# Kernel tuning notes

Measured on AMD Instinct MI355X. Metric: run time of the kernel, lower is better.

Reference implementation:

```python
import jax, jax.numpy as jnp
import numpy as np

D = 1024
H = 16
HD = D // H
N_TEXT = 256
N_VISION = 256
N_FRAMES = 12


def setup_inputs() -> dict:
    key = jax.random.key(0)
    ks = jax.random.split(key, 10)
    s = 1.0 / np.sqrt(D)
    return {
        "text_hidden_states": jax.random.normal(ks[0], (N_TEXT, D), jnp.float32),
        "vision_hidden_states": jax.random.normal(ks[1], (N_VISION, N_FRAMES, D), jnp.float32),
        "wq": jax.random.normal(ks[2], (D, D), jnp.float32) * s,
        "bq": jnp.zeros((D,), jnp.float32),
        "wk": jax.random.normal(ks[3], (D, D), jnp.float32) * s,
        "bk": jnp.zeros((D,), jnp.float32),
        "wv": jax.random.normal(ks[4], (D, D), jnp.float32) * s,
        "bv": jnp.zeros((D,), jnp.float32),
        "wo": jax.random.normal(ks[5], (D, D), jnp.float32) * s,
        "bo": jnp.zeros((D,), jnp.float32),
    }


def reference(text_hidden_states, vision_hidden_states, wq, bq, wk, bk, wv, bv, wo, bo):
    n_text = text_hidden_states.shape[0]
    n_vision, n_frames, _ = vision_hidden_states.shape
    # projections (torch Linear: x @ W.T + b)
    q = (text_hidden_states @ wq.T + bq).reshape(n_text, H, HD)            # [t,h,d]
    k = (vision_hidden_states @ wk.T + bk).reshape(n_vision, n_frames, H, HD)  # [v,f,h,d]
    v = (vision_hidden_states @ wv.T + bv).reshape(n_vision, n_frames, H, HD)  # [v,f,h,d]
    # shared query broadcast over vision batch: scores [v,h,f,t]
    scores = jnp.einsum("vfhd,thd->vhft", k, q) / jnp.sqrt(jnp.asarray(HD, scores_dtype := q.dtype))
    probs = jax.nn.softmax(scores, axis=2)  # softmax over frames (dim=2)
    # attn_output [v,t,h,d] -> [v,t,D]
    out = jnp.einsum("vfhd,vhft->vthd", v, probs).reshape(n_vision, n_text, D)
    return out @ wo.T + bo
```

## Files before the change

### kernel.cpp

```cpp
#include <hip/hip_runtime.h>

typedef short bf16x8 __attribute__((ext_vector_type(8)));
typedef float f32x4 __attribute__((ext_vector_type(4)));

__device__ __forceinline__ unsigned short f2bf(float f) {
  union { float f; unsigned u; } x; x.f = f;
  unsigned u = x.u;
  u += 0x7fffu + ((u >> 16) & 1u);
  return (unsigned short)(u >> 16);
}

__global__ __launch_bounds__(256) void cvt_all(
    const float* __restrict__ text, const float* __restrict__ vis,
    const float* __restrict__ wq, const float* __restrict__ wk,
    const float* __restrict__ wv, const float* __restrict__ wo,
    unsigned short* __restrict__ o0, unsigned short* __restrict__ o1,
    unsigned short* __restrict__ o2, unsigned short* __restrict__ o3,
    unsigned short* __restrict__ o4, unsigned short* __restrict__ o5)
{
  long i4 = (long)blockIdx.x * 256 + threadIdx.x;
  const float* src; unsigned short* dst; long base;
  if      (i4 <   65536) { src = text; dst = o0; base = 0; }
  else if (i4 <  851968) { src = vis;  dst = o1; base = 65536; }
  else if (i4 < 1114112) { src = wq;   dst = o2; base = 851968; }
  else if (i4 < 1376256) { src = wk;   dst = o3; base = 1114112; }
  else if (i4 < 1638400) { src = wv;   dst = o4; base = 1376256; }
  else                   { src = wo;   dst = o5; base = 1638400; }
  long li = i4 - base;
  float4 f = reinterpret_cast<const float4*>(src)[li];
  uint2 u;
  u.x = (unsigned)f2bf(f.x) | ((unsigned)f2bf(f.y) << 16);
  u.y = (unsigned)f2bf(f.z) | ((unsigned)f2bf(f.w) << 16);
  reinterpret_cast<uint2*>(dst)[li] = u;
}

__global__ __launch_bounds__(256) void gemm_abt_bf16(
    const unsigned short* __restrict__ A,
    const unsigned short* __restrict__ B,
    unsigned short* __restrict__ C,
    const float* __restrict__ bias,
    int K, int lda, int ldb, int ldc)
{
  __shared__ unsigned short As[64][40];
  __shared__ unsigned short Bs[64][40];
  const int m0 = blockIdx.y * 64, n0 = blockIdx.x * 64;
  const int tid = threadIdx.x;
  const int lane = tid & 63, w = tid >> 6;
  const int wm = w >> 1, wn = w & 1;
  const int r16 = lane & 15, kg = lane >> 4;
  const int srow = tid >> 2, sseg = tid & 3;

  const f32x4 fzero = {0.f, 0.f, 0.f, 0.f};
  f32x4 acc[2][2];
#pragma unroll
  for (int i = 0; i < 2; ++i)
#pragma unroll
    for (int j = 0; j < 2; ++j) acc[i][j] = fzero;

  for (int k0 = 0; k0 < K; k0 += 32) {
    __syncthreads();
    *reinterpret_cast<int4*>(&As[srow][sseg * 8]) =
        *reinterpret_cast<const int4*>(&A[(long)(m0 + srow) * lda + k0 + sseg * 8]);
    *reinterpret_cast<int4*>(&Bs[srow][sseg * 8]) =
        *reinterpret_cast<const int4*>(&B[(long)(n0 + srow) * ldb + k0 + sseg * 8]);
    __syncthreads();
    bf16x8 a[2], b[2];
#pragma unroll
    for (int i = 0; i < 2; ++i)
      a[i] = *reinterpret_cast<const bf16x8*>(&As[wm * 32 + i * 16 + r16][kg * 8]);
#pragma unroll
    for (int j = 0; j < 2; ++j)
      b[j] = *reinterpret_cast<const bf16x8*>(&Bs[wn * 32 + j * 16 + r16][kg * 8]);
#pragma unroll
    for (int i = 0; i < 2; ++i)
#pragma unroll
      for (int j = 0; j < 2; ++j)
        acc[i][j] = __builtin_amdgcn_mfma_f32_16x16x32_bf16(a[i], b[j], acc[i][j], 0, 0, 0);
  }
#pragma unroll
  for (int i = 0; i < 2; ++i) {
#pragma unroll
    for (int j = 0; j < 2; ++j) {
      const int row = m0 + wm * 32 + i * 16 + kg * 4;
      const int col = n0 + wn * 32 + j * 16 + r16;
      const float bv = bias ? bias[col] : 0.f;
#pragma unroll
      for (int r = 0; r < 4; ++r)
        C[(long)(row + r) * ldc + col] = f2bf(acc[i][j][r] + bv);
    }
  }
}

__global__ __launch_bounds__(256) void gemm_abt_bf16_kv(
    const unsigned short* __restrict__ A,
    const unsigned short* __restrict__ B0,
    const unsigned short* __restrict__ B1,
    unsigned short* __restrict__ C0,
    unsigned short* __restrict__ C1,
    const float* __restrict__ bias0,
    const float* __restrict__ bias1,
    int K, int lda, int ldb, int ldc)
{
  const unsigned short* B = blockIdx.z ? B1 : B0;
  unsigned short* C = blockIdx.z ? C1 : C0;
  const float* bias = blockIdx.z ? bias1 : bias0;

  __shared__ unsigned short As[64][40];
  __shared__ unsigned short Bs[64][40];
  const int m0 = blockIdx.y * 64, n0 = blockIdx.x * 64;
  const int tid = threadIdx.x;
  const int lane = tid & 63, w = tid >> 6;
  const int wm = w >> 1, wn = w & 1;
  const int r16 = lane & 15, kg = lane >> 4;
  const int srow = tid >> 2, sseg = tid & 3;

  const f32x4 fzero = {0.f, 0.f, 0.f, 0.f};
  f32x4 acc[2][2];
#pragma unroll
  for (int i = 0; i < 2; ++i)
#pragma unroll
    for (int j = 0; j < 2; ++j) acc[i][j] = fzero;

  for (int k0 = 0; k0 < K; k0 += 32) {
    __syncthreads();
    *reinterpret_cast<int4*>(&As[srow][sseg * 8]) =
        *reinterpret_cast<const int4*>(&A[(long)(m0 + srow) * lda + k0 + sseg * 8]);
    *reinterpret_cast<int4*>(&Bs[srow][sseg * 8]) =
        *reinterpret_cast<const int4*>(&B[(long)(n0 + srow) * ldb + k0 + sseg * 8]);
    __syncthreads();
    bf16x8 a[2], b[2];
#pragma unroll
    for (int i = 0; i < 2; ++i)
      a[i] = *reinterpret_cast<const bf16x8*>(&As[wm * 32 + i * 16 + r16][kg * 8]);
#pragma unroll
    for (int j = 0; j < 2; ++j)
      b[j] = *reinterpret_cast<const bf16x8*>(&Bs[wn * 32 + j * 16 + r16][kg * 8]);
#pragma unroll
    for (int i = 0; i < 2; ++i)
#pragma unroll
      for (int j = 0; j < 2; ++j)
        acc[i][j] = __builtin_amdgcn_mfma_f32_16x16x32_bf16(a[i], b[j], acc[i][j], 0, 0, 0);
  }
#pragma unroll
  for (int i = 0; i < 2; ++i) {
#pragma unroll
    for (int j = 0; j < 2; ++j) {
      const int row = m0 + wm * 32 + i * 16 + kg * 4;
      const int col = n0 + wn * 32 + j * 16 + r16;
      const float bv = bias ? bias[col] : 0.f;
#pragma unroll
      for (int r = 0; r < 4; ++r)
        C[(long)(row + r) * ldc + col] = f2bf(acc[i][j][r] + bv);
    }
  }
}

__global__ __launch_bounds__(256) void scores_softmax(
    const unsigned short* __restrict__ Kp,
    const unsigned short* __restrict__ Qp,
    unsigned short* __restrict__ P)
{
  const int h = blockIdx.x, v = blockIdx.y;
  const int tid = threadIdx.x, lane = tid & 63, w = tid >> 6;
  const int r16 = lane & 15, kg = lane >> 4;
  __shared__ unsigned short Ks[16][72];
  __shared__ unsigned short Qs[256][72];

  if (tid < 96) {
    const int f = tid >> 3, seg = tid & 7;
    *reinterpret_cast<int4*>(&Ks[f][seg * 8]) =
        *reinterpret_cast<const int4*>(&Kp[(long)(v * 12 + f) * 1024 + h * 64 + seg * 8]);
  } else if (tid < 128) {
    const int f = 12 + ((tid - 96) >> 3), seg = (tid - 96) & 7;
    int4 z; z.x = 0; z.y = 0; z.z = 0; z.w = 0;
    *reinterpret_cast<int4*>(&Ks[f][seg * 8]) = z;
  }
#pragma unroll
  for (int rep = 0; rep < 8; ++rep) {
    const int row = rep * 32 + (tid >> 3), seg = tid & 7;
    *reinterpret_cast<int4*>(&Qs[row][seg * 8]) =
        *reinterpret_cast<const int4*>(&Qp[(long)row * 1024 + h * 64 + seg * 8]);
  }
  __syncthreads();

  const f32x4 fzero = {0.f, 0.f, 0.f, 0.f};
  f32x4 acc[4];
#pragma unroll
  for (int j = 0; j < 4; ++j) acc[j] = fzero;

#pragma unroll
  for (int kk = 0; kk < 64; kk += 32) {
    bf16x8 a = *reinterpret_cast<const bf16x8*>(&Ks[r16][kk + kg * 8]);
#pragma unroll
    for (int j = 0; j < 4; ++j) {
      bf16x8 b = *reinterpret_cast<const bf16x8*>(&Qs[w * 64 + j * 16 + r16][kk + kg * 8]);
      acc[j] = __builtin_amdgcn_mfma_f32_16x16x32_bf16(a, b, acc[j], 0, 0, 0);
    }
  }
#pragma unroll
  for (int j = 0; j < 4; ++j) {
    float lm = -1e30f;
    if (kg < 3) {
#pragma unroll
      for (int r = 0; r < 4; ++r) lm = fmaxf(lm, acc[j][r] * 0.125f);
    }
    lm = fmaxf(lm, __shfl_xor(lm, 16));
    lm = fmaxf(lm, __shfl_xor(lm, 32));
    float p[4]; float ls = 0.f;
    if (kg < 3) {
#pragma unroll
      for (int r = 0; r < 4; ++r) { p[r] = __expf(acc[j][r] * 0.125f - lm); ls += p[r]; }
    }
    ls += __shfl_xor(ls, 16);
    ls += __shfl_xor(ls, 32);
    const float inv = 1.f / ls;
    if (kg < 3) {
      const int t = w * 64 + j * 16 + r16;
#pragma unroll
      for (int r = 0; r < 4; ++r)
        P[((long)v * 256 + t) * 192 + (kg * 4 + r) * 16 + h] = f2bf(p[r] * inv);
    }
  }
}

__global__ __launch_bounds__(256) void combine(
    const unsigned short* __restrict__ VPp,
    const unsigned short* __restrict__ Wo,
    const unsigned short* __restrict__ P,
    const float* __restrict__ bo,
    float* __restrict__ out)
{
  const int wgid = blockIdx.x;
  const int xcd = wgid & 7, idx = wgid >> 3;
  const int v = ((idx & 31) << 3) | xcd;
  const int n0 = (idx >> 5) << 6;

  const int tid = threadIdx.x, lane = tid & 63, w = tid >> 6;
  const int r16 = lane & 15, kg = lane >> 4;

  __shared__ unsigned short BsAll[64 * 192];

  const unsigned short* VPv = VPp + (long)v * 12 * 1024;
#pragma unroll
  for (int hi = 0; hi < 4; ++hi) {
    const int h = (w << 2) + hi;
    const int db = h * 64;
    f32x4 accp[4] = {{0.f,0.f,0.f,0.f},{0.f,0.f,0.f,0.f},{0.f,0.f,0.f,0.f},{0.f,0.f,0.f,0.f}};
#pragma unroll
    for (int kk = 0; kk < 64; kk += 32) {
      bf16x8 a = {0,0,0,0,0,0,0,0};
      if (r16 < 12)
        a = *reinterpret_cast<const bf16x8*>(&VPv[(long)r16 * 1024 + db + kk + kg * 8]);
      bf16x8 bfr[4];
#pragma unroll
      for (int j = 0; j < 4; ++j)
        bfr[j] = *reinterpret_cast<const bf16x8*>(
            &Wo[(long)(n0 + j * 16 + r16) * 1024 + db + kk + kg * 8]);
#pragma unroll
      for (int j = 0; j < 4; ++j)
        accp[j] = __builtin_amdgcn_mfma_f32_16x16x32_bf16(a, bfr[j], accp[j], 0, 0, 0);
    }
#pragma unroll
    for (int j = 0; j < 4; ++j) {
#pragma unroll
      for (int r = 0; r < 4; ++r) {
        const int f = kg * 4 + r;
        if (f < 12) {
          const int o = j * 16 + r16;
          const int k = f * 16 + h;
          BsAll[o * 192 + (((k >> 3) ^ (o & 7)) << 3) + (k & 7)] = f2bf(accp[j][r]);
        }
      }
    }
  }

  const unsigned short* Pv = P + (long)v * 256 * 192;
  bf16x8 aP[4];
#pragma unroll
  for (int i = 0; i < 4; ++i)
    aP[i] = *reinterpret_cast<const bf16x8*>(
        &Pv[(long)(w * 64 + i * 16 + r16) * 192 + kg * 8]);

  __syncthreads();

  f32x4 acc[4][4];
#pragma unroll
  for (int i = 0; i < 4; ++i)
#pragma unroll
    for (int j = 0; j < 4; ++j) { f32x4 z = {0.f,0.f,0.f,0.f}; acc[i][j] = z; }

#pragma unroll
  for (int k0 = 0; k0 < 192; k0 += 32) {
    bf16x8 aC[4];
#pragma unroll
    for (int i = 0; i < 4; ++i) aC[i] = aP[i];
    if (k0 < 160) {
#pragma unroll
      for (int i = 0; i < 4; ++i)
        aP[i] = *reinterpret_cast<const bf16x8*>(
            &Pv[(long)(w * 64 + i * 16 + r16) * 192 + (k0 + 32) + kg * 8]);
    }
    bf16x8 b[4];
#pragma unroll
    for (int j = 0; j < 4; ++j) {
      const int row = j * 16 + r16;
      const int slot = (k0 >> 3) + kg;
      b[j] = *reinterpret_cast<const bf16x8*>(
          &BsAll[row * 192 + ((slot ^ (row & 7)) << 3)]);
    }
#pragma unroll
    for (int i = 0; i < 4; ++i)
#pragma unroll
      for (int j = 0; j < 4; ++j)
        acc[i][j] = __builtin_amdgcn_mfma_f32_16x16x32_bf16(aC[i], b[j], acc[i][j], 0, 0, 0);
  }
#pragma unroll
  for (int i = 0; i < 4; ++i) {
#pragma unroll
    for (int j = 0; j < 4; ++j) {
      const int trow = w * 64 + i * 16 + kg * 4;
      const int col = n0 + j * 16 + r16;
      const float bv = bo[col];
#pragma unroll
      for (int r = 0; r < 4; ++r)
        out[((long)v * 256 + trow + r) * 1024 + col] = acc[i][j][r] + bv;
    }
  }
}

extern "C" void kernel_launch(void* const* d_in, const int* in_sizes, int n_in,
                              void* d_out, int out_size, void* d_ws, size_t ws_size,
                              hipStream_t stream) {
  const float* text = (const float*)d_in[0];
  const float* vis  = (const float*)d_in[1];
  const float* wq   = (const float*)d_in[2];
  const float* bq   = (const float*)d_in[3];
  const float* wk   = (const float*)d_in[4];
  const float* bk   = (const float*)d_in[5];
  const float* wv   = (const float*)d_in[6];
  const float* bv   = (const float*)d_in[7];
  const float* wo   = (const float*)d_in[8];
  const float* bo   = (const float*)d_in[9];
  float* out = (float*)d_out;

  unsigned short* text16 = (unsigned short*)d_ws;
  unsigned short* vis16  = text16 + 262144;
  unsigned short* wq16   = vis16  + 3145728;
  unsigned short* wk16   = wq16   + 1048576;
  unsigned short* wv16   = wk16   + 1048576;
  unsigned short* wo16   = wv16   + 1048576;
  unsigned short* q16    = wo16   + 1048576;
  unsigned short* k16    = q16    + 262144;
  unsigned short* vp16   = k16    + 3145728;
  unsigned short* P      = vp16   + 3145728;

  cvt_all<<<7424, 256, 0, stream>>>(text, vis, wq, wk, wv, wo,
                                    text16, vis16, wq16, wk16, wv16, wo16);
  gemm_abt_bf16<<<dim3(16, 4), 256, 0, stream>>>(text16, wq16, q16, bq, 1024, 1024, 1024, 1024);
  gemm_abt_bf16_kv<<<dim3(16, 48, 2), 256, 0, stream>>>(
      vis16, wk16, wv16, k16, vp16, bk, bv, 1024, 1024, 1024, 1024);
  scores_softmax<<<dim3(16, 256), 256, 0, stream>>>(k16, q16, P);
  combine<<<4096, 256, 0, stream>>>(vp16, wo16, P, bo, out);
}
```

Measured before the change: 273.3 us.

## Split fused combine kernel into Z-projection and output GEMM kernels via workspace

The fused combine kernel is split into two kernels. zh_kernel computes the per-head V·Wo product and writes it to a global Z buffer. out_gemm reloads Z into LDS and multiplies it by P, prefetching the P fragments two stages ahead and storing the output with nontemporal stores. The split is meant to lower register and LDS pressure and raise occupancy in each phase, at the cost of an extra global round-trip for Z (up to 100MB) and a possible chunked loop when the workspace is small.

```diff
diff --git a/kernel.cpp b/kernel.cpp
--- a/kernel.cpp
+++ b/kernel.cpp
@@ -223,17 +223,17 @@
   }
 }
 
-__global__ __launch_bounds__(256) void combine(
+__global__ __launch_bounds__(256) void zh_kernel(
     const unsigned short* __restrict__ VPp,
     const unsigned short* __restrict__ Wo,
-    const unsigned short* __restrict__ P,
-    const float* __restrict__ bo,
-    float* __restrict__ out)
+    unsigned short* __restrict__ Z,
+    int vbase, int vsh)
 {
   const int wgid = blockIdx.x;
   const int xcd = wgid & 7, idx = wgid >> 3;
-  const int v = ((idx & 31) << 3) | xcd;
-  const int n0 = (idx >> 5) << 6;
+  const int vlocal = ((idx & ((1 << vsh) - 1)) << 3) | xcd;
+  const int v = vbase + vlocal;
+  const int n0 = (idx >> vsh) << 6;
 
   const int tid = threadIdx.x, lane = tid & 63, w = tid >> 6;
   const int r16 = lane & 15, kg = lane >> 4;
@@ -273,40 +273,81 @@
       }
     }
   }
-
+  __syncthreads();
+  unsigned short* Zv = Z + ((long)vlocal * 1024 + n0) * 192;
+  const int row = tid >> 2;
+#pragma unroll
+  for (int rep = 0; rep < 6; ++rep) {
+    const int slot = (tid & 3) + (rep << 2);
+    *reinterpret_cast<int4*>(&Zv[(long)row * 192 + slot * 8]) =
+        *reinterpret_cast<const int4*>(&BsAll[row * 192 + ((slot ^ (row & 7)) << 3)]);
+  }
+}
+
+__global__ __launch_bounds__(256) void out_gemm(
+    const unsigned short* __restrict__ Z,
+    const unsigned short* __restrict__ P,
+    const float* __restrict__ bo,
+    float* __restrict__ out,
+    int vbase, int vsh)
+{
+  const int wgid = blockIdx.x;
+  const int xcd = wgid & 7, idx = wgid >> 3;
+  const int vlocal = ((idx & ((1 << vsh) - 1)) << 3) | xcd;
+  const int v = vbase + vlocal;
+  const int n0 = (idx >> vsh) << 6;
+
+  const int tid = threadIdx.x, lane = tid & 63, w = tid >> 6;
+  const int r16 = lane & 15, kg = lane >> 4;
+
+  __shared__ unsigned short Zs[64 * 192];
+
+  const unsigned short* Zv = Z + ((long)vlocal * 1024 + n0) * 192;
+  {
+    const int row = tid >> 2;
+#pragma unroll
+    for (int rep = 0; rep < 6; ++rep) {
+      const int slot = (tid & 3) + (rep << 2);
+      *reinterpret_cast<int4*>(&Zs[row * 192 + ((slot ^ (row & 7)) << 3)]) =
+          *reinterpret_cast<const int4*>(&Zv[(long)row * 192 + slot * 8]);
+    }
+  }
   const unsigned short* Pv = P + (long)v * 256 * 192;
-  bf16x8 aP[4];
+  bf16x8 aP[2][4];
+#pragma unroll
+  for (int s = 0; s < 2; ++s)
+#pragma unroll
+    for (int i = 0; i < 4; ++i)
+      aP[s][i] = *reinterpret_cast<const bf16x8*>(
+          &Pv[(long)(w * 64 + i * 16 + r16) * 192 + s * 32 + kg * 8]);
+
+  __syncthreads();
+
+  f32x4 acc[4][4];
 #pragma unroll
   for (int i = 0; i < 4; ++i)
-    aP[i] = *reinterpret_cast<const bf16x8*>(
-        &Pv[(long)(w * 64 + i * 16 + r16) * 192 + kg * 8]);
-
-  __syncthreads();
-
-  f32x4 acc[4][4];
-#pragma unroll
-  for (int i = 0; i < 4; ++i)
 #pragma unroll
     for (int j = 0; j < 4; ++j) { f32x4 z = {0.f,0.f,0.f,0.f}; acc[i][j] = z; }
 
 #pragma unroll
-  for (int k0 = 0; k0 < 192; k0 += 32) {
-    bf16x8 aC[4];
-#pragma unroll
-    for (int i = 0; i < 4; ++i) aC[i] = aP[i];
-    if (k0 < 160) {
-#pragma unroll
-      for (int i = 0; i < 4; ++i)
-        aP[i] = *reinterpret_cast<const bf16x8*>(
-            &Pv[(long)(w * 64 + i * 16 + r16) * 192 + (k0 + 32) + kg * 8]);
-    }
+  for (int s = 0; s < 6; ++s) {
+    const int k0 = s * 32;
     bf16x8 b[4];
 #pragma unroll
     for (int j = 0; j < 4; ++j) {
       const int row = j * 16 + r16;
       const int slot = (k0 >> 3) + kg;
       b[j] = *reinterpret_cast<const bf16x8*>(
-          &BsAll[row * 192 + ((slot ^ (row & 7)) << 3)]);
+          &Zs[row * 192 + ((slot ^ (row & 7)) << 3)]);
+    }
+    bf16x8 aC[4];
+#pragma unroll
+    for (int i = 0; i < 4; ++i) aC[i] = aP[s & 1][i];
+    if (s < 4) {
+#pragma unroll
+      for (int i = 0; i < 4; ++i)
+        aP[s & 1][i] = *reinterpret_cast<const bf16x8*>(
+            &Pv[(long)(w * 64 + i * 16 + r16) * 192 + (k0 + 64) + kg * 8]);
     }
 #pragma unroll
     for (int i = 0; i < 4; ++i)
@@ -323,7 +364,8 @@
       const float bv = bo[col];
 #pragma unroll
       for (int r = 0; r < 4; ++r)
-        out[((long)v * 256 + trow + r) * 1024 + col] = acc[i][j][r] + bv;
+        __builtin_nontemporal_store(acc[i][j][r] + bv,
+            &out[((long)v * 256 + trow + r) * 1024 + col]);
     }
   }
 }
@@ -353,6 +395,13 @@
   unsigned short* k16    = q16    + 262144;
   unsigned short* vp16   = k16    + 3145728;
   unsigned short* P      = vp16   + 3145728;
+  unsigned short* Zbuf   = P     + 12582912;
+  const size_t base_shorts = 26738688;
+
+  size_t avail_shorts = (ws_size / 2 > base_shorts) ? (ws_size / 2 - base_shorts) : 0;
+  int vchunk = 256;
+  while (vchunk > 8 && (size_t)vchunk * 1024 * 192 > avail_shorts) vchunk >>= 1;
+  int vsh = 0; { int t = vchunk >> 3; while (t > 1) { t >>= 1; ++vsh; } }
 
   cvt_all<<<7424, 256, 0, stream>>>(text, vis, wq, wk, wv, wo,
                                     text16, vis16, wq16, wk16, wv16, wo16);
@@ -360,5 +409,8 @@
   gemm_abt_bf16_kv<<<dim3(16, 48, 2), 256, 0, stream>>>(
       vis16, wk16, wv16, k16, vp16, bk, bv, 1024, 1024, 1024, 1024);
   scores_softmax<<<dim3(16, 256), 256, 0, stream>>>(k16, q16, P);
-  combine<<<4096, 256, 0, stream>>>(vp16, wo16, P, bo, out);
-}
+  for (int vb = 0; vb < 256; vb += vchunk) {
+    zh_kernel<<<16 * vchunk, 256, 0, stream>>>(vp16, wo16, Zbuf, vb, vsh);
+    out_gemm<<<16 * vchunk, 256, 0, stream>>>(Zbuf, P, bo, out, vb, vsh);
+  }
+}
```

Measured after the change: 318.1 us. 1.16x slower.

## Vectorize P stores, double-buffer P loads, stage output through LDS for wide stores

Applied to the files above, without the earlier changes.

Reorders the frame/head index inside the P and staged Wo·V buffers from f*16+h to h*12+f, so each thread's four probabilities are written with one 8-byte store instead of four scattered 2-byte stores. The combine kernel now prefetches P two K-steps ahead using a two-slot register buffer. The epilogue stages accumulators through LDS per wave so it can write output rows as contiguous 16-byte nontemporal stores with vector bias, replacing scalar strided stores. This costs extra LDS traffic, extra registers and a barrier, and it relies on the wave-local staging being correctly ordered by the lgkmcnt waits.

```diff
diff --git a/kernel.cpp b/kernel.cpp
--- a/kernel.cpp
+++ b/kernel.cpp
@@ -216,9 +216,10 @@
     const float inv = 1.f / ls;
     if (kg < 3) {
       const int t = w * 64 + j * 16 + r16;
-#pragma unroll
-      for (int r = 0; r < 4; ++r)
-        P[((long)v * 256 + t) * 192 + (kg * 4 + r) * 16 + h] = f2bf(p[r] * inv);
+      uint2 u2;
+      u2.x = (unsigned)f2bf(p[0] * inv) | ((unsigned)f2bf(p[1] * inv) << 16);
+      u2.y = (unsigned)f2bf(p[2] * inv) | ((unsigned)f2bf(p[3] * inv) << 16);
+      *reinterpret_cast<uint2*>(&P[((long)v * 256 + t) * 192 + h * 12 + kg * 4]) = u2;
     }
   }
 }
@@ -267,7 +268,7 @@
         const int f = kg * 4 + r;
         if (f < 12) {
           const int o = j * 16 + r16;
-          const int k = f * 16 + h;
+          const int k = h * 12 + f;
           BsAll[o * 192 + (((k >> 3) ^ (o & 7)) << 3) + (k & 7)] = f2bf(accp[j][r]);
         }
       }
@@ -275,31 +276,25 @@
   }
 
   const unsigned short* Pv = P + (long)v * 256 * 192;
-  bf16x8 aP[4];
+  bf16x8 aP[2][4];
+#pragma unroll
+  for (int s = 0; s < 2; ++s)
+#pragma unroll
+    for (int i = 0; i < 4; ++i)
+      aP[s][i] = *reinterpret_cast<const bf16x8*>(
+          &Pv[(long)(w * 64 + i * 16 + r16) * 192 + s * 32 + kg * 8]);
+
+  __syncthreads();
+
+  f32x4 acc[4][4];
 #pragma unroll
   for (int i = 0; i < 4; ++i)
-    aP[i] = *reinterpret_cast<const bf16x8*>(
-        &Pv[(long)(w * 64 + i * 16 + r16) * 192 + kg * 8]);
-
-  __syncthreads();
-
-  f32x4 acc[4][4];
-#pragma unroll
-  for (int i = 0; i < 4; ++i)
 #pragma unroll
     for (int j = 0; j < 4; ++j) { f32x4 z = {0.f,0.f,0.f,0.f}; acc[i][j] = z; }
 
 #pragma unroll
-  for (int k0 = 0; k0 < 192; k0 += 32) {
-    bf16x8 aC[4];
-#pragma unroll
-    for (int i = 0; i < 4; ++i) aC[i] = aP[i];
-    if (k0 < 160) {
-#pragma unroll
-      for (int i = 0; i < 4; ++i)
-        aP[i] = *reinterpret_cast<const bf16x8*>(
-            &Pv[(long)(w * 64 + i * 16 + r16) * 192 + (k0 + 32) + kg * 8]);
-    }
+  for (int s = 0; s < 6; ++s) {
+    const int k0 = s * 32;
     bf16x8 b[4];
 #pragma unroll
     for (int j = 0; j < 4; ++j) {
@@ -308,23 +303,47 @@
       b[j] = *reinterpret_cast<const bf16x8*>(
           &BsAll[row * 192 + ((slot ^ (row & 7)) << 3)]);
     }
+    bf16x8 aC[4];
+#pragma unroll
+    for (int i = 0; i < 4; ++i) aC[i] = aP[s & 1][i];
+    if (s < 4) {
+#pragma unroll
+      for (int i = 0; i < 4; ++i)
+        aP[s & 1][i] = *reinterpret_cast<const bf16x8*>(
+            &Pv[(long)(w * 64 + i * 16 + r16) * 192 + (k0 + 64) + kg * 8]);
+    }
 #pragma unroll
     for (int i = 0; i < 4; ++i)
 #pragma unroll
       for (int j = 0; j < 4; ++j)
         acc[i][j] = __builtin_amdgcn_mfma_f32_16x16x32_bf16(aC[i], b[j], acc[i][j], 0, 0, 0);
   }
+
+  __syncthreads();
+  float* Eps = reinterpret_cast<float*>(BsAll);
+  const int c4 = lane & 15;
+  const int rr = lane >> 4;
+  f32x4 bias4 = *reinterpret_cast<const f32x4*>(&bo[n0 + c4 * 4]);
+  const int wbase = w * 1088;
+
 #pragma unroll
   for (int i = 0; i < 4; ++i) {
 #pragma unroll
-    for (int j = 0; j < 4; ++j) {
-      const int trow = w * 64 + i * 16 + kg * 4;
-      const int col = n0 + j * 16 + r16;
-      const float bv = bo[col];
+    for (int j = 0; j < 4; ++j)
 #pragma unroll
       for (int r = 0; r < 4; ++r)
-        out[((long)v * 256 + trow + r) * 1024 + col] = acc[i][j][r] + bv;
-    }
+        Eps[wbase + (kg * 4 + r) * 68 + j * 16 + r16] = acc[i][j][r];
+    asm volatile("s_waitcnt lgkmcnt(0)" ::: "memory");
+#pragma unroll
+    for (int q = 0; q < 4; ++q) {
+      const int row16 = rr + q * 4;
+      f32x4 vle = *reinterpret_cast<const f32x4*>(&Eps[wbase + row16 * 68 + c4 * 4]);
+      vle += bias4;
+      f32x4* dst = reinterpret_cast<f32x4*>(
+          &out[((long)v * 256 + w * 64 + i * 16 + row16) * 1024 + n0 + c4 * 4]);
+      __builtin_nontemporal_store(vle, dst);
+    }
+    asm volatile("s_waitcnt lgkmcnt(0)" ::: "memory");
   }
 }
 
```

New measurement: 231.1 us. 1.18x faster.
